# Kernel tuning notes

Measured on AMD Instinct MI355X. Metric: run time of the kernel, lower is better.

## Reference

```python
import jax, jax.numpy as jnp
import numpy as np

NEG_SLOPE = 0.2
EPS_SOFTMAX = 1e-16
EPS_NORM = 1e-12
H = 4


def gat_conv(x, src, dst, edge_attr, W, att_src, att_dst, W_edge, att_edge, bias, concat):
    """PyG GATConv with edge_dim, add_self_loops=False.
    x: [N, F_in]; src,dst: [E]; edge_attr: [E, edge_dim]
    W: [F_in, H*C]; att_src/att_dst/att_edge: [H, C]; W_edge: [edge_dim, H*C]
    """
    N = x.shape[0]
    C = att_src.shape[1]
    xs = (x @ W).reshape(N, H, C)                      # [N,H,C]
    a_s = jnp.einsum('nhc,hc->nh', xs, att_src)        # [N,H]
    a_d = jnp.einsum('nhc,hc->nh', xs, att_dst)        # [N,H]
    e = (edge_attr @ W_edge).reshape(-1, H, C)         # [E,H,C]
    a_e = jnp.einsum('ehc,hc->eh', e, att_edge)        # [E,H]
    alpha = a_s[src] + a_d[dst] + a_e                  # [E,H]
    alpha = jax.nn.leaky_relu(alpha, NEG_SLOPE)
    # segment softmax over edges grouped by destination node
    m = jax.ops.segment_max(alpha, dst, num_segments=N)        # [N,H]
    ex = jnp.exp(alpha - m[dst])
    denom = jax.ops.segment_sum(ex, dst, num_segments=N)       # [N,H]
    alpha = ex / (denom[dst] + EPS_SOFTMAX)
    # message = attention-weighted source features, scatter-add to dst
    out = jax.ops.segment_sum(xs[src] * alpha[..., None], dst, num_segments=N)  # [N,H,C]
    out = out.reshape(N, H * C) if concat else out.mean(axis=1)
    return out + bias


def l2_normalize(x):
    n = jnp.linalg.norm(x, axis=-1, keepdims=True)
    return x / jnp.maximum(n, EPS_NORM)


def setup_inputs() -> dict:
    key = jax.random.key(0)
    ks = jax.random.split(key, 16)
    N, E, F_in, C1, C2 = 50000, 800000, 128, 64, 64
    glorot = lambda k, shape: jax.random.uniform(
        k, shape, jnp.float32, -1.0, 1.0) * np.sqrt(6.0 / (shape[0] + shape[-1]))
    return {
        'x': jax.random.normal(ks[0], (N, F_in), jnp.float32),
        'edge_index': jax.random.randint(ks[1], (2, E), 0, N, jnp.int32),
        'edge_weight': jax.random.uniform(ks[2], (E, 1), jnp.float32),
        # layer 1: in=128 -> H*C1=256, concat=True
        'W1': glorot(ks[3], (F_in, H * C1)),
        'att_src1': glorot(ks[4], (H, C1)),
        'att_dst1': glorot(ks[5], (H, C1)),
        'We1': glorot(ks[6], (1, H * C1)),
        'att_e1': glorot(ks[7], (H, C1)),
        'b1': jnp.zeros((H * C1,), jnp.float32),
        # layer 2: in=256 -> H*C2, concat=False (mean over heads)
        'W2': glorot(ks[8], (H * C1, H * C2)),
        'att_src2': glorot(ks[9], (H, C2)),
        'att_dst2': glorot(ks[10], (H, C2)),
        'We2': glorot(ks[11], (1, H * C2)),
        'att_e2': glorot(ks[12], (H, C2)),
        'b2': jnp.zeros((C2,), jnp.float32),
    }


def reference(x, edge_index, edge_weight, W1, att_src1, att_dst1, We1, att_e1, b1,
              W2, att_src2, att_dst2, We2, att_e2, b2):
    src, dst = edge_index[0], edge_index[1]
    h = gat_conv(x, src, dst, edge_weight, W1, att_src1, att_dst1, We1, att_e1, b1, concat=True)
    h = jax.nn.relu(l2_normalize(h))
    out = gat_conv(h, src, dst, edge_weight, W2, att_src2, att_dst2, We2, att_e2, b2, concat=False)
    return out
```

## Files before the change

kernel.cpp:

```cpp
#include <hip/hip_runtime.h>
#include <hip/hip_bf16.h>

typedef unsigned short u16;
typedef unsigned long long u64;
using bf16x8 = __attribute__((ext_vector_type(8))) short;
using f32x4v = __attribute__((ext_vector_type(4))) float;
typedef float v2f __attribute__((ext_vector_type(2)));

#define HC 256
#define CDIM 64

__device__ __forceinline__ float b2f(u16 u){
  union { unsigned int i; float f; } c; c.i = ((unsigned)u) << 16; return c.f;
}
__device__ __forceinline__ u16 f2b(float f){
  union { float f; unsigned int i; } c; c.f = f;
  unsigned int x = c.i;
  return (u16)((x + 0x7FFFu + ((x >> 16) & 1u)) >> 16);
}
__device__ __forceinline__ float ldf(const void* p, size_t i, int isbf){
  return isbf ? b2f(((const u16*)p)[i]) : ((const float*)p)[i];
}
__device__ __forceinline__ float sel4(float4 v, int h){ return h==0?v.x:(h==1?v.y:(h==2?v.z:v.w)); }
__device__ __forceinline__ float lrelu(float v){ return v>0.f ? v : 0.2f*v; }

__device__ __forceinline__ void glds16(const void* g, void* l){
  __builtin_amdgcn_global_load_lds(
      (const __attribute__((address_space(1))) unsigned int*)g,
      (__attribute__((address_space(3))) unsigned int*)l, 16, 0, 0);
}

__device__ __forceinline__ float4 wave_max4(float4 m){
  #pragma unroll
  for(int o=32;o>0;o>>=1){
    m.x=fmaxf(m.x,__shfl_xor(m.x,o));
    m.y=fmaxf(m.y,__shfl_xor(m.y,o));
    m.z=fmaxf(m.z,__shfl_xor(m.z,o));
    m.w=fmaxf(m.w,__shfl_xor(m.w,o));
  }
  return m;
}
__device__ __forceinline__ float4 wave_sum4(float4 m){
  #pragma unroll
  for(int o=32;o>0;o>>=1){
    m.x+=__shfl_xor(m.x,o);
    m.y+=__shfl_xor(m.y,o);
    m.z+=__shfl_xor(m.z,o);
    m.w+=__shfl_xor(m.w,o);
  }
  return m;
}

__global__ void k_hist(const int* __restrict__ dst, int E, int N, int* __restrict__ deg,
                       int* __restrict__ rank,
                       const u16* __restrict__ x, int nelem, int* __restrict__ flag){
  int e = blockIdx.x*256 + threadIdx.x;
  if (e < E){
    int d = dst[e];
    if ((unsigned)d < (unsigned)N) rank[e] = atomicAdd(&deg[d], 1);
  }
  if (blockIdx.x == 0){
    __shared__ int bad;
    if (threadIdx.x==0) bad = 0;
    __syncthreads();
    int n = nelem < 8192 ? nelem : 8192;
    int localbad = 0;
    for (int i=threadIdx.x; i<n; i+=256){
      int ex = (x[i] >> 7) & 0xFF;
      if (ex >= 140) localbad++;
    }
    if (localbad) atomicAdd(&bad, 1);
    __syncthreads();
    if (threadIdx.x==0) *flag = (bad==0) ? 1 : 0;
  }
}

__global__ void k_scan1(const int* __restrict__ in, int* __restrict__ out, int* __restrict__ bsums, int n){
  __shared__ int s[256];
  int t = threadIdx.x;
  int i = blockIdx.x*256 + t;
  int v = (i<n)? in[i] : 0;
  s[t]=v; __syncthreads();
  for(int off=1; off<256; off<<=1){
    int tv = (t>=off)? s[t-off] : 0;
    __syncthreads();
    s[t]+=tv; __syncthreads();
  }
  if (i<n) out[i] = s[t]-v;
  if (t==255) bsums[blockIdx.x] = s[255];
}

__global__ void k_scan2(int* __restrict__ bsums, int nb){
  __shared__ int s[256];
  int t=threadIdx.x;
  int v=(t<nb)? bsums[t]:0;
  s[t]=v; __syncthreads();
  for(int off=1; off<256; off<<=1){
    int tv=(t>=off)? s[t-off]:0;
    __syncthreads();
    s[t]+=tv; __syncthreads();
  }
  if (t<nb) bsums[t]=s[t]-v;
}

__global__ void k_scatter(const int* __restrict__ src, const int* __restrict__ dst,
                          const void* __restrict__ ew, int E, int N,
                          const int* __restrict__ rowptr, const int* __restrict__ bsums,
                          const int* __restrict__ rank, u64* __restrict__ epk,
                          const int* __restrict__ flagp){
  int e = blockIdx.x*256+threadIdx.x;
  if (e>=E) return;
  int bf = *flagp;
  int d = dst[e];
  if ((unsigned)d >= (unsigned)N) return;
  int p = rowptr[d] + bsums[d>>8] + rank[e];
  int s = src[e];
  if ((unsigned)s >= (unsigned)N) s = 0;
  u64 v = ((u64)__float_as_uint(ldf(ew, e, bf)) << 32) | (unsigned)s;
  __builtin_nontemporal_store(v, &epk[p]);
}

__global__ void k_prep(const void* __restrict__ W1, const void* __restrict__ W2,
                       const void* __restrict__ We1, const void* __restrict__ ae1,
                       const void* __restrict__ We2, const void* __restrict__ ae2,
                       u16* __restrict__ Bt1, u16* __restrict__ Bt2, float* __restrict__ ce,
                       const int* __restrict__ flagp){
  int bf = *flagp;
  int b = blockIdx.x, t = threadIdx.x;
  if (b < 128){
    Bt1[(size_t)t*128 + b] = f2b(ldf(W1, (size_t)b*HC + t, bf));
  } else if (b < 384){
    int k = b - 128;
    Bt2[(size_t)t*256 + k] = f2b(ldf(W2, (size_t)k*HC + t, bf));
  } else {
    float p1 = ldf(We1, t, bf)*ldf(ae1, t, bf);
    float p2 = ldf(We2, t, bf)*ldf(ae2, t, bf);
    #pragma unroll
    for(int o=32;o>0;o>>=1){ p1+=__shfl_xor(p1,o); p2+=__shfl_xor(p2,o); }
    if((t&63)==0){ ce[t>>6]=p1; ce[4+(t>>6)]=p2; }
  }
}

__global__ __launch_bounds__(256) void k_gemm_mfma(
    const void* __restrict__ A, int a_ext, const u16* __restrict__ Bt,
    u16* __restrict__ C, const void* __restrict__ att_s, const void* __restrict__ att_d,
    float* __restrict__ a_s, float* __restrict__ a_d,
    int M, int K, const int* __restrict__ flagp)
{
  __shared__ u16 sh[64*264];
  __shared__ float att_sh[512];
  u16* As = sh;
  u16* Bs = sh + 2048;
  int bf = *flagp;
  int a_bf = a_ext ? bf : 1;
  int tid = threadIdx.x;
  int lane = tid & 63, w = tid >> 6;
  int quad = lane >> 4, ln = lane & 15;
  int m0 = blockIdx.x * 64;

  att_sh[tid]       = ldf(att_s, tid, bf);
  att_sh[256 + tid] = ldf(att_d, tid, bf);

  f32x4v acc[4][4] = {};
  for (int k0 = 0; k0 < K; k0 += 32){
    if (!a_ext){
      const u16* gA = (const u16*)A + (size_t)(m0 + (tid>>2))*K + k0 + (size_t)(tid&3)*8;
      glds16(gA, (char*)As + (size_t)w*1024);
    } else {
      int m = tid >> 2, g = tid & 3;
      int r = m0 + m;
      uint4 pack;
      if (r < M){
        size_t base = (size_t)r*K + k0 + g*8;
        if (a_bf){
          pack = *(const uint4*)((const u16*)A + base);
        } else {
          const float* Af = (const float*)A + base;
          float4 f0 = *(const float4*)Af;
          float4 f1 = *(const float4*)(Af+4);
          unsigned a0 = (unsigned)f2b(f0.x) | ((unsigned)f2b(f0.y)<<16);
          unsigned a1 = (unsigned)f2b(f0.z) | ((unsigned)f2b(f0.w)<<16);
          unsigned a2 = (unsigned)f2b(f1.x) | ((unsigned)f2b(f1.y)<<16);
          unsigned a3 = (unsigned)f2b(f1.z) | ((unsigned)f2b(f1.w)<<16);
          pack = make_uint4(a0,a1,a2,a3);
        }
      } else pack = make_uint4(0,0,0,0);
      ((uint4*)As)[tid] = pack;
    }
    #pragma unroll
    for (int i=0;i<4;i++){
      const u16* gB = Bt + (size_t)(i*64 + (tid>>2))*K + k0 + (size_t)(tid&3)*8;
      glds16(gB, (char*)Bs + (size_t)i*4096 + (size_t)w*1024);
    }
    __syncthreads();
    bf16x8 af[4], bfr[4];
    #pragma unroll
    for (int mi=0;mi<4;mi++) af[mi] = *(const bf16x8*)&As[(mi*16+ln)*32 + quad*8];
    #pragma unroll
    for (int nj=0;nj<4;nj++) bfr[nj] = *(const bf16x8*)&Bs[((size_t)w*64+nj*16+ln)*32 + quad*8];
    #pragma unroll
    for (int mi=0;mi<4;mi++)
      #pragma unroll
      for (int nj=0;nj<4;nj++)
        acc[mi][nj] = __builtin_amdgcn_mfma_f32_16x16x32_bf16(af[mi], bfr[nj], acc[mi][nj], 0,0,0);
    __syncthreads();
  }
  #pragma unroll
  for (int mi=0;mi<4;mi++)
    #pragma unroll
    for (int nj=0;nj<4;nj++){
      union { __hip_bfloat162 h2; u16 u[2]; } cv0, cv1;
      cv0.h2 = __float22bfloat162_rn(make_float2(acc[mi][nj][0], acc[mi][nj][1]));
      cv1.h2 = __float22bfloat162_rn(make_float2(acc[mi][nj][2], acc[mi][nj][3]));
      int col = w*64 + nj*16 + ln;
      int rbase = mi*16 + quad*4;
      sh[(rbase+0)*264 + col] = cv0.u[0];
      sh[(rbase+1)*264 + col] = cv0.u[1];
      sh[(rbase+2)*264 + col] = cv1.u[0];
      sh[(rbase+3)*264 + col] = cv1.u[1];
    }
  __syncthreads();
  #pragma unroll
  for (int j=0;j<8;j++){
    int idx = j*256 + tid;
    int r = idx >> 5, gq = idx & 31;
    if (m0 + r < M)
      *(uint4*)(C + (size_t)(m0+r)*HC + gq*8) = *(const uint4*)&sh[r*264 + gq*8];
  }
  {
    int r  = w*16 + ln;
    int hh = quad;
    const u16* crow = &sh[r*264 + hh*64];
    const float* asv = &att_sh[hh*64];
    const float* adv = &att_sh[256 + hh*64];
    float ps = 0.f, pd = 0.f;
    #pragma unroll
    for (int cb=0; cb<64; cb+=8){
      ushort4 ua = *(const ushort4*)&crow[cb];
      ushort4 ub = *(const ushort4*)&crow[cb+4];
      float4 sa = *(const float4*)&asv[cb];
      float4 sb = *(const float4*)&asv[cb+4];
      float4 da = *(const float4*)&adv[cb];
      float4 db = *(const float4*)&adv[cb+4];
      float c0=b2f(ua.x), c1=b2f(ua.y), c2=b2f(ua.z), c3=b2f(ua.w);
      float c4=b2f(ub.x), c5=b2f(ub.y), c6=b2f(ub.z), c7=b2f(ub.w);
      ps += c0*sa.x + c1*sa.y + c2*sa.z + c3*sa.w + c4*sb.x + c5*sb.y + c6*sb.z + c7*sb.w;
      pd += c0*da.x + c1*da.y + c2*da.z + c3*da.w + c4*db.x + c5*db.y + c6*db.z + c7*db.w;
    }
    if (m0 + r < M){
      a_s[(size_t)(m0+r)*4 + hh] = ps;
      a_d[(size_t)(m0+r)*4 + hh] = pd;
    }
  }
}

__global__ __launch_bounds__(256) void k_soft_agg(
    const u16* __restrict__ xs, const int* __restrict__ rowptr, const int* __restrict__ bsums,
    const int* __restrict__ deg, const u64* __restrict__ epk,
    const float* __restrict__ a_s, const float* __restrict__ a_d, const float* __restrict__ ce4,
    const void* __restrict__ bias, void* __restrict__ outp, int N, int layer,
    const int* __restrict__ flagp){
  int bf = *flagp;
  int lane = threadIdx.x & 63;
  int w = threadIdx.x >> 6;
  int n = (blockIdx.x<<2) + w;
  if (n >= N) return;
  int row = rowptr[n] + bsums[n>>8];
  int dg = deg[n];
  float4 ad = *(const float4*)&a_d[(size_t)n*4];
  float4 ce = *(const float4*)ce4;
  int h = lane >> 4;
  float4 acc = make_float4(0.f,0.f,0.f,0.f);
  if (dg > 0){
    if (dg <= 64){
      int   s_reg = 0;
      float4 ar = make_float4(-1e30f,-1e30f,-1e30f,-1e30f);
      if (lane < dg){
        u64 pk = epk[row + lane];
        int s = (int)(unsigned)(pk & 0xFFFFFFFFull);
        if ((unsigned)s >= (unsigned)N) s = 0;
        s_reg = s;
        float wv = __uint_as_float((unsigned)(pk >> 32));
        float4 as = *(const float4*)&a_s[(size_t)s*4];
        ar.x = lrelu(as.x+ad.x+wv*ce.x);
        ar.y = lrelu(as.y+ad.y+wv*ce.y);
        ar.z = lrelu(as.z+ad.z+wv*ce.z);
        ar.w = lrelu(as.w+ad.w+wv*ce.w);
      }
      float4 m = wave_max4(ar);
      float4 ex = make_float4(0.f,0.f,0.f,0.f);
      if (lane < dg){
        ex.x=__expf(ar.x-m.x); ex.y=__expf(ar.y-m.y);
        ex.z=__expf(ar.z-m.z); ex.w=__expf(ar.w-m.w);
      }
      float4 ss = wave_sum4(ex);
      float4 wgt;
      wgt.x = ex.x/(ss.x+1e-16f); wgt.y = ex.y/(ss.y+1e-16f);
      wgt.z = ex.z/(ss.z+1e-16f); wgt.w = ex.w/(ss.w+1e-16f);
      float tw[4];
      #pragma unroll
      for (int j=0;j<4;j++){
        if (j*16 < dg){
          int srcl = j*16 + (lane & 15);
          float c0=__shfl(wgt.x,srcl), c1=__shfl(wgt.y,srcl);
          float c2=__shfl(wgt.z,srcl), c3=__shfl(wgt.w,srcl);
          tw[j] = (h==0)?c0:((h==1)?c1:((h==2)?c2:c3));
        } else tw[j] = 0.f;
      }
      int ibase = lane & 48;
      v2f a01 = {0.f,0.f}, a23 = {0.f,0.f};
      #pragma unroll
      for (int j=0;j<4;j++){
        int j0 = j*16;
        if (j0 >= dg) break;
        float twj = tw[j];
        int cnt = dg - j0; if (cnt > 16) cnt = 16;
        int t = 0;
        for (; t+4<=cnt; t+=4){
          int e = j0 + t;
          int s0=__builtin_amdgcn_readlane(s_reg,e+0);
          int s1=__builtin_amdgcn_readlane(s_reg,e+1);
          int s2=__builtin_amdgcn_readlane(s_reg,e+2);
          int s3=__builtin_amdgcn_readlane(s_reg,e+3);
          float w0=__shfl(twj, ibase+t+0);
          float w1=__shfl(twj, ibase+t+1);
          float w2=__shfl(twj, ibase+t+2);
          float w3=__shfl(twj, ibase+t+3);
          uint2 x0 = *(const uint2*)&xs[(size_t)s0*HC + lane*4];
          uint2 x1 = *(const uint2*)&xs[(size_t)s1*HC + lane*4];
          uint2 x2 = *(const uint2*)&xs[(size_t)s2*HC + lane*4];
          uint2 x3 = *(const uint2*)&xs[(size_t)s3*HC + lane*4];
          v2f f;
          f = (v2f){__uint_as_float(x0.x<<16), __uint_as_float(x0.x&0xFFFF0000u)}; a01 += f*w0;
          f = (v2f){__uint_as_float(x0.y<<16), __uint_as_float(x0.y&0xFFFF0000u)}; a23 += f*w0;
          f = (v2f){__uint_as_float(x1.x<<16), __uint_as_float(x1.x&0xFFFF0000u)}; a01 += f*w1;
          f = (v2f){__uint_as_float(x1.y<<16), __uint_as_float(x1.y&0xFFFF0000u)}; a23 += f*w1;
          f = (v2f){__uint_as_float(x2.x<<16), __uint_as_float(x2.x&0xFFFF0000u)}; a01 += f*w2;
          f = (v2f){__uint_as_float(x2.y<<16), __uint_as_float(x2.y&0xFFFF0000u)}; a23 += f*w2;
          f = (v2f){__uint_as_float(x3.x<<16), __uint_as_float(x3.x&0xFFFF0000u)}; a01 += f*w3;
          f = (v2f){__uint_as_float(x3.y<<16), __uint_as_float(x3.y&0xFFFF0000u)}; a23 += f*w3;
        }
        for (; t<cnt; t++){
          int s0=__builtin_amdgcn_readlane(s_reg,j0+t);
          float w0=__shfl(twj, ibase+t);
          uint2 x0 = *(const uint2*)&xs[(size_t)s0*HC + lane*4];
          v2f f;
          f = (v2f){__uint_as_float(x0.x<<16), __uint_as_float(x0.x&0xFFFF0000u)}; a01 += f*w0;
          f = (v2f){__uint_as_float(x0.y<<16), __uint_as_float(x0.y&0xFFFF0000u)}; a23 += f*w0;
        }
      }
      acc.x = a01.x; acc.y = a01.y; acc.z = a23.x; acc.w = a23.y;
    } else {
      float4 m = make_float4(-1e30f,-1e30f,-1e30f,-1e30f);
      for (int p=lane;p<dg;p+=64){
        u64 pk = epk[row+p];
        int s = (int)(unsigned)(pk & 0xFFFFFFFFull);
        if ((unsigned)s >= (unsigned)N) s = 0;
        float wv = __uint_as_float((unsigned)(pk >> 32));
        float4 as = *(const float4*)&a_s[(size_t)s*4];
        m.x=fmaxf(m.x, lrelu(as.x+ad.x+wv*ce.x));
        m.y=fmaxf(m.y, lrelu(as.y+ad.y+wv*ce.y));
        m.z=fmaxf(m.z, lrelu(as.z+ad.z+wv*ce.z));
        m.w=fmaxf(m.w, lrelu(as.w+ad.w+wv*ce.w));
      }
      m = wave_max4(m);
      float4 ss = make_float4(0.f,0.f,0.f,0.f);
      for (int p=lane;p<dg;p+=64){
        u64 pk = epk[row+p];
        int s = (int)(unsigned)(pk & 0xFFFFFFFFull);
        if ((unsigned)s >= (unsigned)N) s = 0;
        float wv = __uint_as_float((unsigned)(pk >> 32));
        float4 as = *(const float4*)&a_s[(size_t)s*4];
        ss.x+=__expf(lrelu(as.x+ad.x+wv*ce.x)-m.x);
        ss.y+=__expf(lrelu(as.y+ad.y+wv*ce.y)-m.y);
        ss.z+=__expf(lrelu(as.z+ad.z+wv*ce.z)-m.z);
        ss.w+=__expf(lrelu(as.w+ad.w+wv*ce.w)-m.w);
      }
      ss = wave_sum4(ss);
      float rsel=1.f/(sel4(ss,h)+1e-16f), mh=sel4(m,h), adh=sel4(ad,h), ceh=sel4(ce,h);
      for (int e=0;e<dg;e++){
        u64 pk = epk[row+e];
        int s = (int)(unsigned)(pk & 0xFFFFFFFFull);
        if ((unsigned)s >= (unsigned)N) s = 0;
        float wv = __uint_as_float((unsigned)(pk >> 32));
        float arv = lrelu(a_s[(size_t)s*4+h]+adh+wv*ceh);
        float wgt = __expf(arv-mh)*rsel;
        ushort4 xv4 = *(const ushort4*)&xs[(size_t)s*HC + lane*4];
        acc.x+=wgt*b2f(xv4.x); acc.y+=wgt*b2f(xv4.y);
        acc.z+=wgt*b2f(xv4.z); acc.w+=wgt*b2f(xv4.w);
      }
    }
  }
  if (layer==1){
    float4 v;
    v.x = acc.x + ldf(bias, lane*4+0, bf);
    v.y = acc.y + ldf(bias, lane*4+1, bf);
    v.z = acc.z + ldf(bias, lane*4+2, bf);
    v.w = acc.w + ldf(bias, lane*4+3, bf);
    float ss = v.x*v.x+v.y*v.y+v.z*v.z+v.w*v.w;
    #pragma unroll
    for(int o=32;o>0;o>>=1) ss += __shfl_xor(ss,o);
    float inv = 1.f/fmaxf(sqrtf(ss), 1e-12f);
    ushort4 o4;
    o4.x = f2b(fmaxf(v.x*inv,0.f)); o4.y = f2b(fmaxf(v.y*inv,0.f));
    o4.z = f2b(fmaxf(v.z*inv,0.f)); o4.w = f2b(fmaxf(v.w*inv,0.f));
    *(ushort4*)((u16*)outp + (size_t)n*HC + lane*4) = o4;
  } else {
    float4 s = acc;
    #pragma unroll
    for (int o=16;o<=32;o<<=1){
      s.x+=__shfl_xor(s.x,o); s.y+=__shfl_xor(s.y,o);
      s.z+=__shfl_xor(s.z,o); s.w+=__shfl_xor(s.w,o);
    }
    if (lane < 16){
      float4 v;
      v.x = 0.25f*s.x + ldf(bias, lane*4+0, bf);
      v.y = 0.25f*s.y + ldf(bias, lane*4+1, bf);
      v.z = 0.25f*s.z + ldf(bias, lane*4+2, bf);
      v.w = 0.25f*s.w + ldf(bias, lane*4+3, bf);
      if (bf){
        ushort4 o4; o4.x=f2b(v.x); o4.y=f2b(v.y); o4.z=f2b(v.z); o4.w=f2b(v.w);
        *(ushort4*)((u16*)outp + (size_t)n*CDIM + lane*4) = o4;
      } else {
        *(float4*)((float*)outp + (size_t)n*CDIM + lane*4) = v;
      }
    }
  }
}

extern "C" void kernel_launch(void* const* d_in, const int* in_sizes, int n_in,
                              void* d_out, int out_size, void* d_ws, size_t ws_size,
                              hipStream_t stream){
  const void* x_in = d_in[0];
  const int* eidx  = (const int*)d_in[1];
  const void* ew   = d_in[2];
  const void* W1   = d_in[3];
  const void* as1  = d_in[4];
  const void* ad1  = d_in[5];
  const void* We1  = d_in[6];
  const void* ae1  = d_in[7];
  const void* b1   = d_in[8];
  const void* W2   = d_in[9];
  const void* as2  = d_in[10];
  const void* ad2  = d_in[11];
  const void* We2  = d_in[12];
  const void* ae2  = d_in[13];
  const void* b2   = d_in[14];

  int N = in_sizes[0]/128;
  int E = in_sizes[2];
  const int* src = eidx;
  const int* dst = eidx + E;

  char* w = (char*)d_ws;
  auto alloc = [&](size_t bytes)->char*{ char* p=w; w += (bytes+255)/256*256; return p; };
  int*   flag  = (int*)alloc(256);
  u16*   xs    = (u16*)alloc((size_t)N*HC*2);
  u16*   agg   = (u16*)alloc((size_t)N*HC*2);
  float* a_s   = (float*)alloc((size_t)N*4*4);
  float* a_d   = (float*)alloc((size_t)N*4*4);
  int*   deg   = (int*)alloc((size_t)N*4);
  int*   rowptr= (int*)alloc((size_t)N*4);
  int*   bsums = (int*)alloc(256*4);
  int*   rank  = (int*)alloc((size_t)E*4);
  u64*   epk   = (u64*)alloc((size_t)E*8);
  float* ce    = (float*)alloc(256);
  u16*   Bt1   = (u16*)alloc((size_t)HC*128*2);
  u16*   Bt2   = (u16*)alloc((size_t)HC*HC*2);

  (void)hipMemsetAsync(deg, 0, (size_t)N*4, stream);

  int eb = (E+255)/256;
  int nb = (N+255)/256;
  k_hist<<<eb,256,0,stream>>>(dst, E, N, deg, rank, (const u16*)x_in, in_sizes[0], flag);
  k_scan1<<<nb,256,0,stream>>>(deg, rowptr, bsums, N);
  k_scan2<<<1,256,0,stream>>>(bsums, nb);
  k_scatter<<<eb,256,0,stream>>>(src, dst, ew, E, N, rowptr, bsums, rank, epk, flag);
  k_prep<<<385,256,0,stream>>>(W1, W2, We1, ae1, We2, ae2, Bt1, Bt2, ce, flag);

  int gemmBlocks = (N+63)/64;
  int nwb = (N+3)/4;

  k_gemm_mfma<<<gemmBlocks,256,0,stream>>>(x_in, 1, Bt1, xs, as1, ad1, a_s, a_d, N, 128, flag);
  k_soft_agg<<<nwb,256,0,stream>>>(xs, rowptr, bsums, deg, epk, a_s, a_d, ce, b1, agg, N, 1, flag);

  k_gemm_mfma<<<gemmBlocks,256,0,stream>>>(agg, 0, Bt2, xs, as2, ad2, a_s, a_d, N, 256, flag);
  k_soft_agg<<<nwb,256,0,stream>>>(xs, rowptr, bsums, deg, epk, a_s, a_d, ce+4, b2, d_out, N, 2, flag);
}
```

Before: 341.5 us.

## Stage edge indices and weights in LDS and software-pipeline gathers in soft_agg

For nodes with degree at most 64, the per-wave softmax reductions now skip shuffle stages that cannot hold valid lanes, based on the degree. Source indices and per-head weights are written to LDS instead of being redistributed with readlane and shfl. The aggregation loop keeps a rotating buffer of 8 in-flight row gathers, prefetching the next batch while accumulating the current one, to hide memory latency. This adds LDS use and registers, which may lower occupancy.

```diff
diff --git a/kernel.cpp b/kernel.cpp
--- a/kernel.cpp
+++ b/kernel.cpp
@@ -260,6 +260,8 @@
     const float* __restrict__ a_s, const float* __restrict__ a_d, const float* __restrict__ ce4,
     const void* __restrict__ bias, void* __restrict__ outp, int N, int layer,
     const int* __restrict__ flagp){
+  __shared__ int   lds_s[4][64];
+  __shared__ float lds_w[4][64][4];
   int bf = *flagp;
   int lane = threadIdx.x & 63;
   int w = threadIdx.x >> 6;
@@ -287,66 +289,75 @@
         ar.z = lrelu(as.z+ad.z+wv*ce.z);
         ar.w = lrelu(as.w+ad.w+wv*ce.w);
       }
-      float4 m = wave_max4(ar);
+      float4 m = ar;
+      if (dg > 32){
+        m.x=fmaxf(m.x,__shfl_xor(m.x,32)); m.y=fmaxf(m.y,__shfl_xor(m.y,32));
+        m.z=fmaxf(m.z,__shfl_xor(m.z,32)); m.w=fmaxf(m.w,__shfl_xor(m.w,32));
+      }
+      if (dg > 16){
+        m.x=fmaxf(m.x,__shfl_xor(m.x,16)); m.y=fmaxf(m.y,__shfl_xor(m.y,16));
+        m.z=fmaxf(m.z,__shfl_xor(m.z,16)); m.w=fmaxf(m.w,__shfl_xor(m.w,16));
+      }
+      #pragma unroll
+      for(int o=8;o>0;o>>=1){
+        m.x=fmaxf(m.x,__shfl_xor(m.x,o)); m.y=fmaxf(m.y,__shfl_xor(m.y,o));
+        m.z=fmaxf(m.z,__shfl_xor(m.z,o)); m.w=fmaxf(m.w,__shfl_xor(m.w,o));
+      }
       float4 ex = make_float4(0.f,0.f,0.f,0.f);
       if (lane < dg){
         ex.x=__expf(ar.x-m.x); ex.y=__expf(ar.y-m.y);
         ex.z=__expf(ar.z-m.z); ex.w=__expf(ar.w-m.w);
       }
-      float4 ss = wave_sum4(ex);
+      float4 ss = ex;
+      if (dg > 32){
+        ss.x+=__shfl_xor(ss.x,32); ss.y+=__shfl_xor(ss.y,32);
+        ss.z+=__shfl_xor(ss.z,32); ss.w+=__shfl_xor(ss.w,32);
+      }
+      if (dg > 16){
+        ss.x+=__shfl_xor(ss.x,16); ss.y+=__shfl_xor(ss.y,16);
+        ss.z+=__shfl_xor(ss.z,16); ss.w+=__shfl_xor(ss.w,16);
+      }
+      #pragma unroll
+      for(int o=8;o>0;o>>=1){
+        ss.x+=__shfl_xor(ss.x,o); ss.y+=__shfl_xor(ss.y,o);
+        ss.z+=__shfl_xor(ss.z,o); ss.w+=__shfl_xor(ss.w,o);
+      }
       float4 wgt;
       wgt.x = ex.x/(ss.x+1e-16f); wgt.y = ex.y/(ss.y+1e-16f);
       wgt.z = ex.z/(ss.z+1e-16f); wgt.w = ex.w/(ss.w+1e-16f);
-      float tw[4];
-      #pragma unroll
-      for (int j=0;j<4;j++){
-        if (j*16 < dg){
-          int srcl = j*16 + (lane & 15);
-          float c0=__shfl(wgt.x,srcl), c1=__shfl(wgt.y,srcl);
-          float c2=__shfl(wgt.z,srcl), c3=__shfl(wgt.w,srcl);
-          tw[j] = (h==0)?c0:((h==1)?c1:((h==2)?c2:c3));
-        } else tw[j] = 0.f;
-      }
-      int ibase = lane & 48;
+      if (lane < dg){
+        lds_s[w][lane] = s_reg;
+        *(float4*)&lds_w[w][lane][0] = wgt;
+      }
       v2f a01 = {0.f,0.f}, a23 = {0.f,0.f};
-      #pragma unroll
-      for (int j=0;j<4;j++){
-        int j0 = j*16;
-        if (j0 >= dg) break;
-        float twj = tw[j];
-        int cnt = dg - j0; if (cnt > 16) cnt = 16;
-        int t = 0;
-        for (; t+4<=cnt; t+=4){
-          int e = j0 + t;
-          int s0=__builtin_amdgcn_readlane(s_reg,e+0);
-          int s1=__builtin_amdgcn_readlane(s_reg,e+1);
-          int s2=__builtin_amdgcn_readlane(s_reg,e+2);
-          int s3=__builtin_amdgcn_readlane(s_reg,e+3);
-          float w0=__shfl(twj, ibase+t+0);
-          float w1=__shfl(twj, ibase+t+1);
-          float w2=__shfl(twj, ibase+t+2);
-          float w3=__shfl(twj, ibase+t+3);
-          uint2 x0 = *(const uint2*)&xs[(size_t)s0*HC + lane*4];
-          uint2 x1 = *(const uint2*)&xs[(size_t)s1*HC + lane*4];
-          uint2 x2 = *(const uint2*)&xs[(size_t)s2*HC + lane*4];
-          uint2 x3 = *(const uint2*)&xs[(size_t)s3*HC + lane*4];
-          v2f f;
-          f = (v2f){__uint_as_float(x0.x<<16), __uint_as_float(x0.x&0xFFFF0000u)}; a01 += f*w0;
-          f = (v2f){__uint_as_float(x0.y<<16), __uint_as_float(x0.y&0xFFFF0000u)}; a23 += f*w0;
-          f = (v2f){__uint_as_float(x1.x<<16), __uint_as_float(x1.x&0xFFFF0000u)}; a01 += f*w1;
-          f = (v2f){__uint_as_float(x1.y<<16), __uint_as_float(x1.y&0xFFFF0000u)}; a23 += f*w1;
-          f = (v2f){__uint_as_float(x2.x<<16), __uint_as_float(x2.x&0xFFFF0000u)}; a01 += f*w2;
-          f = (v2f){__uint_as_float(x2.y<<16), __uint_as_float(x2.y&0xFFFF0000u)}; a23 += f*w2;
-          f = (v2f){__uint_as_float(x3.x<<16), __uint_as_float(x3.x&0xFFFF0000u)}; a01 += f*w3;
-          f = (v2f){__uint_as_float(x3.y<<16), __uint_as_float(x3.y&0xFFFF0000u)}; a23 += f*w3;
+      uint2 xb[8]; float wb[8];
+      {
+        int pre = dg < 8 ? dg : 8;
+        #pragma unroll
+        for (int k=0;k<8;k++){
+          if (k < pre){
+            int s0 = lds_s[w][k];
+            wb[k]  = lds_w[w][k][h];
+            xb[k]  = *(const uint2*)&xs[(size_t)s0*HC + lane*4];
+          }
         }
-        for (; t<cnt; t++){
-          int s0=__builtin_amdgcn_readlane(s_reg,j0+t);
-          float w0=__shfl(twj, ibase+t);
-          uint2 x0 = *(const uint2*)&xs[(size_t)s0*HC + lane*4];
-          v2f f;
-          f = (v2f){__uint_as_float(x0.x<<16), __uint_as_float(x0.x&0xFFFF0000u)}; a01 += f*w0;
-          f = (v2f){__uint_as_float(x0.y<<16), __uint_as_float(x0.y&0xFFFF0000u)}; a23 += f*w0;
+      }
+      for (int base=0; base<dg; base+=8){
+        int mcnt = dg - base; if (mcnt > 8) mcnt = 8;
+        #pragma unroll
+        for (int k=0;k<8;k++){
+          if (k < mcnt){
+            uint2 xv = xb[k]; float wk = wb[k];
+            int nk = base + 8 + k;
+            if (nk < dg){
+              int s0 = lds_s[w][nk];
+              wb[k]  = lds_w[w][nk][h];
+              xb[k]  = *(const uint2*)&xs[(size_t)s0*HC + lane*4];
+            }
+            v2f f;
+            f = (v2f){__uint_as_float(xv.x<<16), __uint_as_float(xv.x&0xFFFF0000u)}; a01 += f*wk;
+            f = (v2f){__uint_as_float(xv.y<<16), __uint_as_float(xv.y&0xFFFF0000u)}; a23 += f*wk;
+          }
         }
       }
       acc.x = a01.x; acc.y = a01.y; acc.z = a23.x; acc.w = a23.y;
```

After: 361.6 us. +5.9%, slower.
